# Performance work log

Hardware: AMD Instinct MI355X
Metric: run time of the kernel (lower is better)

The kernel has to match this reference:

```python
import jax, jax.numpy as jnp
import numpy as np

N = 65536   # total nodes
E = 1048576 # total edges (avg degree 16)
B = 512     # graphs in batch
H = 4       # gat1 heads
C = 64      # per-head channels / GNN_HIDDEN


def segment_softmax(logits, seg, num_segments):
    # numerically stable softmax over segments (PyG softmax semantics, eps=1e-16)
    m = jax.ops.segment_max(logits, seg, num_segments=num_segments)
    m = jnp.where(jnp.isfinite(m), m, 0.0)
    e = jnp.exp(logits - m[seg])
    s = jax.ops.segment_sum(e, seg, num_segments=num_segments)
    return e / (s[seg] + 1e-16)


def gat_conv(x, edge_index, edge_attr, W, att_src, att_dst, We, att_edge, bias, heads, out_ch, concat):
    # PyG GATConv with edge_dim, add_self_loops=False
    n = x.shape[0]
    h = (x @ W).reshape(n, heads, out_ch)                 # (N,H,C)
    src, dst = edge_index[0], edge_index[1]
    a_s = jnp.sum(h * att_src, axis=-1)                   # (N,H)
    a_d = jnp.sum(h * att_dst, axis=-1)                   # (N,H)
    he = (edge_attr @ We).reshape(-1, heads, out_ch)      # (E,H,C)
    a_e = jnp.sum(he * att_edge, axis=-1)                 # (E,H)
    alpha = jax.nn.leaky_relu(a_s[src] + a_d[dst] + a_e, negative_slope=0.2)
    alpha = segment_softmax(alpha, dst, n)                # softmax over incoming edges per dst
    out = jax.ops.segment_sum(h[src] * alpha[..., None], dst, num_segments=n)  # (N,H,C)
    out = out.reshape(n, heads * out_ch) if concat else out.mean(axis=1)
    return out + bias


def setup_inputs() -> dict:
    key = jax.random.key(0)
    ks = jax.random.split(key, 24)
    s = 0.05
    d = {}
    d["global_feat"] = jax.random.normal(ks[0], (B, 512), jnp.float32)
    d["x"] = jax.random.normal(ks[1], (N, 13), jnp.float32)
    d["roi_feats"] = jax.random.normal(ks[2], (N, 256), jnp.float32)
    d["edge_index"] = jax.random.randint(ks[3], (2, E), 0, N)
    d["edge_attr"] = jax.random.normal(ks[4], (E, 5), jnp.float32)
    d["batch_vec"] = jnp.sort(jax.random.randint(ks[5], (N,), 0, B))
    # roi_proj / scene_proj
    d["roi_W"] = jax.random.normal(ks[6], (256, 64), jnp.float32) * s
    d["roi_b"] = jnp.zeros((64,), jnp.float32)
    d["scene_W"] = jax.random.normal(ks[7], (512, 128), jnp.float32) * s
    d["scene_b"] = jnp.zeros((128,), jnp.float32)
    d["g1_W"] = jax.random.normal(ks[8], (77, H * C), jnp.float32) * s
    d["g1_att_src"] = jax.random.normal(ks[9], (H, C), jnp.float32) * s
    d["g1_att_dst"] = jax.random.normal(ks[10], (H, C), jnp.float32) * s
    d["g1_We"] = jax.random.normal(ks[11], (5, H * C), jnp.float32) * s
    d["g1_att_edge"] = jax.random.normal(ks[12], (H, C), jnp.float32) * s
    d["g1_bias"] = jnp.zeros((H * C,), jnp.float32)
    # gat2: 256 -> 64, 1 head
    d["g2_W"] = jax.random.normal(ks[13], (H * C, C), jnp.float32) * s
    d["g2_att_src"] = jax.random.normal(ks[14], (1, C), jnp.float32) * s
    d["g2_att_dst"] = jax.random.normal(ks[15], (1, C), jnp.float32) * s
    d["g2_We"] = jax.random.normal(ks[16], (5, C), jnp.float32) * s
    d["g2_att_edge"] = jax.random.normal(ks[17], (1, C), jnp.float32) * s
    d["g2_bias"] = jnp.zeros((C,), jnp.float32)
    # attention pooling gate + classifier
    d["gate_W"] = jax.random.normal(ks[18], (C, 1), jnp.float32) * s
    d["gate_b"] = jnp.zeros((1,), jnp.float32)
    d["cls1_W"] = jax.random.normal(ks[19], (128 + C, 64), jnp.float32) * s
    d["cls1_b"] = jnp.zeros((64,), jnp.float32)
    d["cls2_W"] = jax.random.normal(ks[20], (64, 3), jnp.float32) * s
    d["cls2_b"] = jnp.zeros((3,), jnp.float32)
    return d


def reference(global_feat, x, roi_feats, edge_index, edge_attr, batch_vec,
              roi_W, roi_b, scene_W, scene_b,
              g1_W, g1_att_src, g1_att_dst, g1_We, g1_att_edge, g1_bias,
              g2_W, g2_att_src, g2_att_dst, g2_We, g2_att_edge, g2_bias,
              gate_W, gate_b, cls1_W, cls1_b, cls2_W, cls2_b):
    scene = global_feat @ scene_W + scene_b                       # (B,128)
    vis = jax.nn.relu(roi_feats @ roi_W + roi_b)                  # (N,64)
    h = jnp.concatenate([x, vis], axis=-1)                        # (N,77)
    h = jax.nn.relu(gat_conv(h, edge_index, edge_attr, g1_W, g1_att_src, g1_att_dst, g1_We, g1_att_edge, g1_bias, H, C, True))
    h = gat_conv(h, edge_index, edge_attr, g2_W, g2_att_src, g2_att_dst, g2_We, g2_att_edge, g2_bias, 1, C, False)  # (N,64)
    # GlobalAttention pooling
    gate = segment_softmax((h @ gate_W + gate_b)[:, 0], batch_vec, B)
    rel = jax.ops.segment_sum(gate[:, None] * h, batch_vec, num_segments=B)  # (B,64)
    comb = jnp.concatenate([scene, rel], axis=-1)                 # (B,192)
    hid = jax.nn.relu(comb @ cls1_W + cls1_b)                     # dropout off (eval)
    return hid @ cls2_W + cls2_b                                  # (B,3)
```

## Files before the change

kernel.cpp:

```cpp
#include <hip/hip_runtime.h>

#define N_NODES 65536
#define N_EDGES 1048576
#define NB      512

typedef unsigned short u16;
typedef unsigned int   u32;
typedef unsigned long long u64;

__device__ __forceinline__ float bf2f(u16 u) { return __uint_as_float(((u32)u) << 16); }
__device__ __forceinline__ float lo16(u32 u) { return __uint_as_float(u << 16); }
__device__ __forceinline__ float hi16(u32 u) { return __uint_as_float(u & 0xffff0000u); }
__device__ __forceinline__ u16 f2bf(float f) {
    u32 u = __float_as_uint(f);
    u32 r = (u + 0x7fffu + ((u >> 16) & 1u)) >> 16;
    return (u16)r;
}
__device__ __forceinline__ float wsum(float v) {
    for (int o = 32; o; o >>= 1) v += __shfl_xor(v, o, 64);
    return v;
}
__device__ __forceinline__ float wmax(float v) {
    for (int o = 32; o; o >>= 1) v = fmaxf(v, __shfl_xor(v, o, 64));
    return v;
}

__global__ void k_prep(const float* g1We, const float* g1ae, const float* g2We, const float* g2ae,
                       float* M1, float* M2) {
    int t = threadIdx.x;
    if (t < 20) {
        int j = t >> 2, h = t & 3;
        float s = 0.f;
        for (int c = 0; c < 64; c++) s += g1We[j * 256 + h * 64 + c] * g1ae[h * 64 + c];
        M1[t] = s;
    } else if (t < 25) {
        int j = t - 20;
        float s = 0.f;
        for (int c = 0; c < 64; c++) s += g2We[j * 64 + c] * g2ae[c];
        M2[j] = s;
    }
}

__global__ __launch_bounds__(256) void k_scene(const float* __restrict__ gf, const float* __restrict__ W,
                                               const float* __restrict__ bias, float* __restrict__ scene) {
    int idx = blockIdx.x * 256 + threadIdx.x;
    int b = idx >> 7, j = idx & 127;
    float acc = 0.f;
    for (int k = 0; k < 512; k++) acc += gf[b * 512 + k] * W[k * 128 + j];
    scene[idx] = acc + bias[j];
}

__global__ __launch_bounds__(256) void k_hist(const int* ei, int* cnt) {
    int e = blockIdx.x * 256 + threadIdx.x;
    atomicAdd(&cnt[ei[N_EDGES + e]], 1);
}

__global__ __launch_bounds__(256) void k_scan_blk(const int* __restrict__ cnt, int* __restrict__ pre,
                                                  int* __restrict__ bsum) {
    __shared__ int sd[256];
    int t = threadIdx.x, b = blockIdx.x;
    int base = b * 1024 + t * 4;
    int4 c = *(const int4*)(cnt + base);
    int s = c.x + c.y + c.z + c.w;
    sd[t] = s;
    __syncthreads();
    for (int off = 1; off < 256; off <<= 1) {
        int v = (t >= off) ? sd[t - off] : 0;
        __syncthreads();
        sd[t] += v;
        __syncthreads();
    }
    int excl = sd[t] - s;
    int4 p;
    p.x = excl;
    p.y = excl + c.x;
    p.z = excl + c.x + c.y;
    p.w = excl + c.x + c.y + c.z;
    *(int4*)(pre + base) = p;
    if (t == 255) bsum[b] = sd[255];
}

__global__ __launch_bounds__(64) void k_scan_top(int* bsum) {
    int t = threadIdx.x;
    int v = bsum[t];
    int inc = v;
    for (int off = 1; off < 64; off <<= 1) {
        int u = __shfl_up(inc, off, 64);
        if (t >= off) inc += u;
    }
    bsum[t] = inc - v;
}

__global__ __launch_bounds__(256) void k_scan_fix(const int* __restrict__ pre, const int* __restrict__ bsum,
                                                  int* __restrict__ row_ptr, int* __restrict__ coarse_cur) {
    int i = blockIdx.x * 256 + threadIdx.x;
    int v = pre[i] + bsum[i >> 10];
    row_ptr[i] = v;
    if ((i & 255) == 0) coarse_cur[i >> 8] = v;
    if (i == 0) row_ptr[N_NODES] = N_EDGES;
}

__global__ __launch_bounds__(256) void k_bucket(const int* __restrict__ ei, int* coarse_cur,
                                                u32* __restrict__ bpack, int* __restrict__ bsrc) {
    __shared__ u32 stageP[4096];
    __shared__ int stageS[4096];
    __shared__ int bcnt[256], bscan[256], boff[256], gbase[256];
    int t = threadIdx.x;
    int e0 = blockIdx.x * 4096;
    bcnt[t] = 0;
    __syncthreads();
    int dreg[16], sreg[16];
    for (int it = 0; it < 16; it++) {
        int e = e0 + it * 256 + t;
        int dd = ei[N_EDGES + e];
        dreg[it] = dd;
        sreg[it] = ei[e];
        atomicAdd(&bcnt[dd >> 8], 1);
    }
    __syncthreads();
    int v = bcnt[t];
    bscan[t] = v;
    __syncthreads();
    for (int off = 1; off < 256; off <<= 1) {
        int u = (t >= off) ? bscan[t - off] : 0;
        __syncthreads();
        bscan[t] += u;
        __syncthreads();
    }
    boff[t] = bscan[t] - v;
    gbase[t] = v ? atomicAdd(&coarse_cur[t], v) : 0;
    __syncthreads();
    for (int it = 0; it < 16; it++) {
        int e = e0 + it * 256 + t;
        int b = dreg[it] >> 8;
        int pos = atomicAdd(&boff[b], 1);
        stageP[pos] = ((u32)e << 12) | (u32)(dreg[it] & 255);
        stageS[pos] = sreg[it];
    }
    __syncthreads();
    for (int idx = t; idx < 4096; idx += 256) {
        int lo = 0, hi = 255;
        while (lo < hi) { int mid = (lo + hi) >> 1; if (bscan[mid] > idx) hi = mid; else lo = mid + 1; }
        int b = lo;
        int g = gbase[b] + (idx - (bscan[b] - bcnt[b]));
        bpack[g] = stageP[idx];
        bsrc[g] = stageS[idx];
    }
}

__global__ __launch_bounds__(256) void k_sortb(const u32* __restrict__ bpack, const int* __restrict__ bsrc,
                                               const int* __restrict__ row_ptr,
                                               int* __restrict__ eord, int* __restrict__ ssrc) {
    __shared__ int cur[256];
    int t = threadIdx.x, b = blockIdx.x;
    int nbase = b * 256;
    cur[t] = row_ptr[nbase + t];
    __syncthreads();
    int beg = row_ptr[nbase];
    int end = row_ptr[nbase + 256];
    for (int i = beg + t; i < end; i += 256) {
        u32 wd = bpack[i];
        int src = bsrc[i];
        int d8 = wd & 255;
        int pos = atomicAdd(&cur[d8], 1);
        eord[pos] = (int)(wd >> 12);
        ssrc[pos] = src;
    }
}

__global__ __launch_bounds__(256) void k_payload(const int* __restrict__ eord, const float* __restrict__ ea,
                                                 const float* __restrict__ M1, const float* __restrict__ M2,
                                                 float* __restrict__ a1es, float* __restrict__ a2es) {
    int pos = blockIdx.x * 256 + threadIdx.x;
    int e = eord[pos];
    float v[5];
    for (int j = 0; j < 5; j++) v[j] = ea[(size_t)e * 5 + j];
    float4 o;
    o.x = v[0]*M1[0]  + v[1]*M1[4]  + v[2]*M1[8]  + v[3]*M1[12] + v[4]*M1[16];
    o.y = v[0]*M1[1]  + v[1]*M1[5]  + v[2]*M1[9]  + v[3]*M1[13] + v[4]*M1[17];
    o.z = v[0]*M1[2]  + v[1]*M1[6]  + v[2]*M1[10] + v[3]*M1[14] + v[4]*M1[18];
    o.w = v[0]*M1[3]  + v[1]*M1[7]  + v[2]*M1[11] + v[3]*M1[15] + v[4]*M1[19];
    *(float4*)(a1es + (size_t)pos * 4) = o;
    a2es[pos] = v[0]*M2[0] + v[1]*M2[1] + v[2]*M2[2] + v[3]*M2[3] + v[4]*M2[4];
}

__global__ __launch_bounds__(256) void k_vis(const float* __restrict__ A, const float* __restrict__ W,
                                             const float* __restrict__ bias, float* __restrict__ out) {
    __shared__ float At[64][68];
    __shared__ float Wl[64][68];
    int t = threadIdx.x;
    int n0 = blockIdx.x * 64;
    int cg = t & 15, rg = t >> 4;
    int sr = t >> 2, scs = (t & 3) * 16;
    float acc[4][4];
    for (int i = 0; i < 4; i++) for (int j = 0; j < 4; j++) acc[i][j] = 0.f;
    for (int kc = 0; kc < 4; kc++) {
        __syncthreads();
        const float* ap = A + (size_t)(n0 + sr) * 256 + kc * 64 + scs;
        float4 q0 = *(const float4*)ap, q1 = *(const float4*)(ap + 4);
        float4 q2 = *(const float4*)(ap + 8), q3 = *(const float4*)(ap + 12);
        At[scs + 0][sr] = q0.x;  At[scs + 1][sr] = q0.y;  At[scs + 2][sr] = q0.z;  At[scs + 3][sr] = q0.w;
        At[scs + 4][sr] = q1.x;  At[scs + 5][sr] = q1.y;  At[scs + 6][sr] = q1.z;  At[scs + 7][sr] = q1.w;
        At[scs + 8][sr] = q2.x;  At[scs + 9][sr] = q2.y;  At[scs + 10][sr] = q2.z; At[scs + 11][sr] = q2.w;
        At[scs + 12][sr] = q3.x; At[scs + 13][sr] = q3.y; At[scs + 14][sr] = q3.z; At[scs + 15][sr] = q3.w;
        const float* wp = W + (size_t)(kc * 64 + sr) * 64 + scs;
        *(float4*)&Wl[sr][scs + 0]  = *(const float4*)wp;
        *(float4*)&Wl[sr][scs + 4]  = *(const float4*)(wp + 4);
        *(float4*)&Wl[sr][scs + 8]  = *(const float4*)(wp + 8);
        *(float4*)&Wl[sr][scs + 12] = *(const float4*)(wp + 12);
        __syncthreads();
        for (int k = 0; k < 64; k++) {
            float4 a4 = *(const float4*)&At[k][rg * 4];
            float4 w4 = *(const float4*)&Wl[k][cg * 4];
            acc[0][0] += a4.x * w4.x; acc[0][1] += a4.x * w4.y; acc[0][2] += a4.x * w4.z; acc[0][3] += a4.x * w4.w;
            acc[1][0] += a4.y * w4.x; acc[1][1] += a4.y * w4.y; acc[1][2] += a4.y * w4.z; acc[1][3] += a4.y * w4.w;
            acc[2][0] += a4.z * w4.x; acc[2][1] += a4.z * w4.y; acc[2][2] += a4.z * w4.z; acc[2][3] += a4.z * w4.w;
            acc[3][0] += a4.w * w4.x; acc[3][1] += a4.w * w4.y; acc[3][2] += a4.w * w4.z; acc[3][3] += a4.w * w4.w;
        }
    }
    float4 bb = *(const float4*)(bias + cg * 4);
    for (int i = 0; i < 4; i++) {
        float4 o;
        o.x = fmaxf(acc[i][0] + bb.x, 0.f);
        o.y = fmaxf(acc[i][1] + bb.y, 0.f);
        o.z = fmaxf(acc[i][2] + bb.z, 0.f);
        o.w = fmaxf(acc[i][3] + bb.w, 0.f);
        *(float4*)(out + (size_t)(n0 + rg * 4 + i) * 64 + cg * 4) = o;
    }
}

__global__ __launch_bounds__(256) void k_h2(const u16* __restrict__ A, const float* __restrict__ W,
                                            u16* __restrict__ out) {
    __shared__ float At[64][68];
    __shared__ float Wl[64][68];
    int t = threadIdx.x;
    int n0 = blockIdx.x * 64;
    int cg = t & 15, rg = t >> 4;
    int sr = t >> 2, scs = (t & 3) * 16;
    float acc[4][4];
    for (int i = 0; i < 4; i++) for (int j = 0; j < 4; j++) acc[i][j] = 0.f;
    for (int kc = 0; kc < 4; kc++) {
        __syncthreads();
        const u16* ap = A + (size_t)(n0 + sr) * 256 + kc * 64 + scs;
        uint4 u0 = *(const uint4*)ap;
        uint4 u1 = *(const uint4*)(ap + 8);
        At[scs + 0][sr] = lo16(u0.x);  At[scs + 1][sr] = hi16(u0.x);
        At[scs + 2][sr] = lo16(u0.y);  At[scs + 3][sr] = hi16(u0.y);
        At[scs + 4][sr] = lo16(u0.z);  At[scs + 5][sr] = hi16(u0.z);
        At[scs + 6][sr] = lo16(u0.w);  At[scs + 7][sr] = hi16(u0.w);
        At[scs + 8][sr] = lo16(u1.x);  At[scs + 9][sr] = hi16(u1.x);
        At[scs + 10][sr] = lo16(u1.y); At[scs + 11][sr] = hi16(u1.y);
        At[scs + 12][sr] = lo16(u1.z); At[scs + 13][sr] = hi16(u1.z);
        At[scs + 14][sr] = lo16(u1.w); At[scs + 15][sr] = hi16(u1.w);
        const float* wp = W + (size_t)(kc * 64 + sr) * 64 + scs;
        *(float4*)&Wl[sr][scs + 0]  = *(const float4*)wp;
        *(float4*)&Wl[sr][scs + 4]  = *(const float4*)(wp + 4);
        *(float4*)&Wl[sr][scs + 8]  = *(const float4*)(wp + 8);
        *(float4*)&Wl[sr][scs + 12] = *(const float4*)(wp + 12);
        __syncthreads();
        for (int k = 0; k < 64; k++) {
            float4 a4 = *(const float4*)&At[k][rg * 4];
            float4 w4 = *(const float4*)&Wl[k][cg * 4];
            acc[0][0] += a4.x * w4.x; acc[0][1] += a4.x * w4.y; acc[0][2] += a4.x * w4.z; acc[0][3] += a4.x * w4.w;
            acc[1][0] += a4.y * w4.x; acc[1][1] += a4.y * w4.y; acc[1][2] += a4.y * w4.z; acc[1][3] += a4.y * w4.w;
            acc[2][0] += a4.z * w4.x; acc[2][1] += a4.z * w4.y; acc[2][2] += a4.z * w4.z; acc[2][3] += a4.z * w4.w;
            acc[3][0] += a4.w * w4.x; acc[3][1] += a4.w * w4.y; acc[3][2] += a4.w * w4.z; acc[3][3] += a4.w * w4.w;
        }
    }
    u32* outu = (u32*)out;
    for (int i = 0; i < 4; i++) {
        uint2 pk;
        pk.x = (u32)f2bf(acc[i][0]) | ((u32)f2bf(acc[i][1]) << 16);
        pk.y = (u32)f2bf(acc[i][2]) | ((u32)f2bf(acc[i][3]) << 16);
        *(uint2*)(outu + (size_t)(n0 + rg * 4 + i) * 32 + cg * 2) = pk;
    }
}

__global__ __launch_bounds__(256) void k_h1(const float* __restrict__ x, const float* __restrict__ vis,
                                            const float* __restrict__ g1W, u16* __restrict__ h1) {
    __shared__ float At[77][36];
    __shared__ float Wl[77][132];
    int t = threadIdx.x, ch = blockIdx.y;
    int n0 = blockIdx.x * 32;
    int cg = t & 31, rg = t >> 5;
    for (int idx = t; idx < 9856; idx += 256) {
        int k = idx >> 7, c = idx & 127;
        Wl[k][c] = g1W[(size_t)k * 256 + ch * 128 + c];
    }
    for (int idx = t; idx < 2464; idx += 256) {
        int r = idx / 77, k = idx - r * 77;
        At[k][r] = (k < 13) ? x[(size_t)(n0 + r) * 13 + k] : vis[(size_t)(n0 + r) * 64 + (k - 13)];
    }
    __syncthreads();
    float acc[4][4];
    for (int i = 0; i < 4; i++) for (int j = 0; j < 4; j++) acc[i][j] = 0.f;
    for (int k = 0; k < 77; k++) {
        float4 a4 = *(const float4*)&At[k][rg * 4];
        float4 w4 = *(const float4*)&Wl[k][cg * 4];
        acc[0][0] += a4.x * w4.x; acc[0][1] += a4.x * w4.y; acc[0][2] += a4.x * w4.z; acc[0][3] += a4.x * w4.w;
        acc[1][0] += a4.y * w4.x; acc[1][1] += a4.y * w4.y; acc[1][2] += a4.y * w4.z; acc[1][3] += a4.y * w4.w;
        acc[2][0] += a4.z * w4.x; acc[2][1] += a4.z * w4.y; acc[2][2] += a4.z * w4.z; acc[2][3] += a4.z * w4.w;
        acc[3][0] += a4.w * w4.x; acc[3][1] += a4.w * w4.y; acc[3][2] += a4.w * w4.z; acc[3][3] += a4.w * w4.w;
    }
    for (int i = 0; i < 4; i++) {
        uint2 pk;
        pk.x = (u32)f2bf(acc[i][0]) | ((u32)f2bf(acc[i][1]) << 16);
        pk.y = (u32)f2bf(acc[i][2]) | ((u32)f2bf(acc[i][3]) << 16);
        *(uint2*)(h1 + (size_t)(n0 + rg * 4 + i) * 256 + ch * 128 + cg * 4) = pk;
    }
}

__global__ __launch_bounds__(256) void k_a1(const u16* __restrict__ h1, const float* __restrict__ as_,
                                            const float* __restrict__ ad_, float* a1s, float* a1d) {
    int t = threadIdx.x;
    int w = t >> 6, L = t & 63;
    float4 as4 = *(const float4*)(as_ + 4 * L);
    float4 ad4 = *(const float4*)(ad_ + 4 * L);
    int base = (blockIdx.x * 4 + w) * 16;
    for (int j = 0; j < 16; j++) {
        int n = base + j;
        uint2 u = *((const uint2*)(h1 + (size_t)n * 256) + L);
        float v0 = lo16(u.x), v1 = hi16(u.x), v2 = lo16(u.y), v3 = hi16(u.y);
        float ps = v0 * as4.x + v1 * as4.y + v2 * as4.z + v3 * as4.w;
        float pd = v0 * ad4.x + v1 * ad4.y + v2 * ad4.z + v3 * ad4.w;
        for (int o = 1; o < 16; o <<= 1) { ps += __shfl_xor(ps, o, 64); pd += __shfl_xor(pd, o, 64); }
        if ((L & 15) == 0) {
            a1s[n * 4 + (L >> 4)] = ps;
            a1d[n * 4 + (L >> 4)] = pd;
        }
    }
}

__global__ __launch_bounds__(256) void k_a2(const u16* __restrict__ h2b, const float* __restrict__ as_,
                                            const float* __restrict__ ad_, float* a2s, float* a2d) {
    int t = threadIdx.x;
    int w = t >> 6, lane = t & 63;
    int n = blockIdx.x * 4 + w;
    float v = bf2f(h2b[(size_t)n * 64 + lane]);
    float ps = wsum(v * as_[lane]);
    float pd = wsum(v * ad_[lane]);
    if (lane == 0) { a2s[n] = ps; a2d[n] = pd; }
}

__global__ __launch_bounds__(256) void k_soft1(const int* __restrict__ row_ptr, const int* __restrict__ ssrc,
                                               const float* __restrict__ a1s, const float* __restrict__ a1d,
                                               const float* __restrict__ a1es, float* __restrict__ w1) {
    int t = threadIdx.x;
    int wv = t >> 6, L = t & 63;
    int n = blockIdx.x * 4 + wv;
    int h = L >> 4, j = L & 15;
    int beg = row_ptr[n], deg = row_ptr[n + 1] - beg;
    if (deg == 0) return;
    float adn = a1d[n * 4 + h];
    float m = -3.0e38f, s = 0.f;
    for (int i = j; i < deg; i += 16) {
        int pos = beg + i;
        float l = a1s[ssrc[pos] * 4 + h] + adn + a1es[(size_t)pos * 4 + h];
        l = (l > 0.f) ? l : 0.2f * l;
        if (l > m) { s = s * __expf(m - l) + 1.f; m = l; }
        else       { s += __expf(l - m); }
    }
    for (int o = 1; o < 16; o <<= 1) {
        float mo = __shfl_xor(m, o, 64), so = __shfl_xor(s, o, 64);
        float M = fmaxf(m, mo);
        s = s * __expf(m - M) + so * __expf(mo - M);
        m = M;
    }
    float inv = 1.f / (s + 1e-16f);
    for (int i = j; i < deg; i += 16) {
        int pos = beg + i;
        float l = a1s[ssrc[pos] * 4 + h] + adn + a1es[(size_t)pos * 4 + h];
        l = (l > 0.f) ? l : 0.2f * l;
        w1[(size_t)pos * 4 + h] = __expf(l - m) * inv;
    }
}

__global__ __launch_bounds__(256) void k_gath1(const int* __restrict__ row_ptr, const int* __restrict__ ssrc,
                                               const float* __restrict__ w1, const u16* __restrict__ h1,
                                               const float* __restrict__ bias, u16* __restrict__ out1) {
    int t = threadIdx.x;
    int wv = t >> 6, L = t & 63;
    int n = blockIdx.x * 4 + wv;
    int beg = row_ptr[n], deg = row_ptr[n + 1] - beg;
    int halfE = L >> 5;
    int L32 = L & 31;
    int hd = L32 >> 3;
    float acc[8];
    #pragma unroll
    for (int j = 0; j < 8; j++) acc[j] = 0.f;
    int last = beg + deg - 1;
    for (int i = 0; i < deg; i += 4) {
        int iA = i + halfE, iB = i + 2 + halfE;
        int pA = beg + iA, pB = beg + iB;
        bool vA = iA < deg, vB = iB < deg;
        int cA = vA ? pA : last, cB = vB ? pB : last;
        int sA = ssrc[cA], sB = ssrc[cB];
        float wA = vA ? w1[(size_t)cA * 4 + hd] : 0.f;
        float wB = vB ? w1[(size_t)cB * 4 + hd] : 0.f;
        uint4 uA = *((const uint4*)(h1 + (size_t)sA * 256) + L32);
        uint4 uB = *((const uint4*)(h1 + (size_t)sB * 256) + L32);
        acc[0] += wA * lo16(uA.x) + wB * lo16(uB.x);
        acc[1] += wA * hi16(uA.x) + wB * hi16(uB.x);
        acc[2] += wA * lo16(uA.y) + wB * lo16(uB.y);
        acc[3] += wA * hi16(uA.y) + wB * hi16(uB.y);
        acc[4] += wA * lo16(uA.z) + wB * lo16(uB.z);
        acc[5] += wA * hi16(uA.z) + wB * hi16(uB.z);
        acc[6] += wA * lo16(uA.w) + wB * lo16(uB.w);
        acc[7] += wA * hi16(uA.w) + wB * hi16(uB.w);
    }
    #pragma unroll
    for (int j = 0; j < 8; j++) acc[j] += __shfl_xor(acc[j], 32, 64);
    if (halfE == 0) {
        float4 b0 = *(const float4*)(bias + 8 * L32);
        float4 b1 = *(const float4*)(bias + 8 * L32 + 4);
        uint4 pk;
        pk.x = (u32)f2bf(fmaxf(acc[0] + b0.x, 0.f)) | ((u32)f2bf(fmaxf(acc[1] + b0.y, 0.f)) << 16);
        pk.y = (u32)f2bf(fmaxf(acc[2] + b0.z, 0.f)) | ((u32)f2bf(fmaxf(acc[3] + b0.w, 0.f)) << 16);
        pk.z = (u32)f2bf(fmaxf(acc[4] + b1.x, 0.f)) | ((u32)f2bf(fmaxf(acc[5] + b1.y, 0.f)) << 16);
        pk.w = (u32)f2bf(fmaxf(acc[6] + b1.z, 0.f)) | ((u32)f2bf(fmaxf(acc[7] + b1.w, 0.f)) << 16);
        *((uint4*)(out1 + (size_t)n * 256) + L32) = pk;
    }
}

__global__ __launch_bounds__(256) void k_soft2(const int* __restrict__ row_ptr, const int* __restrict__ ssrc,
                                               const float* __restrict__ a2s, const float* __restrict__ a2d,
                                               const float* __restrict__ a2es, float* __restrict__ w2) {
    int t = threadIdx.x;
    int wv = t >> 6, L = t & 63;
    int g = L >> 4, j = L & 15;
    int n = blockIdx.x * 16 + wv * 4 + g;
    int beg = row_ptr[n], deg = row_ptr[n + 1] - beg;
    if (deg == 0) return;
    float adn = a2d[n];
    float m = -3.0e38f, s = 0.f;
    for (int i = j; i < deg; i += 16) {
        int pos = beg + i;
        float l = a2s[ssrc[pos]] + adn + a2es[pos];
        l = (l > 0.f) ? l : 0.2f * l;
        if (l > m) { s = s * __expf(m - l) + 1.f; m = l; }
        else       { s += __expf(l - m); }
    }
    for (int o = 1; o < 16; o <<= 1) {
        float mo = __shfl_xor(m, o, 64), so = __shfl_xor(s, o, 64);
        float M = fmaxf(m, mo);
        s = s * __expf(m - M) + so * __expf(mo - M);
        m = M;
    }
    float inv = 1.f / (s + 1e-16f);
    for (int i = j; i < deg; i += 16) {
        int pos = beg + i;
        float l = a2s[ssrc[pos]] + adn + a2es[pos];
        l = (l > 0.f) ? l : 0.2f * l;
        w2[pos] = __expf(l - m) * inv;
    }
}

__global__ __launch_bounds__(256) void k_gath2(const int* __restrict__ row_ptr, const int* __restrict__ ssrc,
                                               const float* __restrict__ w2, const u16* __restrict__ h2b,
                                               const float* __restrict__ bias, float* __restrict__ hfin) {
    int t = threadIdx.x;
    int wv = t >> 6, L = t & 63;
    int n = blockIdx.x * 4 + wv;
    int beg = row_ptr[n], deg = row_ptr[n + 1] - beg;
    int halfE = L >> 5;
    int L32 = L & 31;
    float a0 = 0.f, a1v = 0.f;
    int last = beg + deg - 1;
    const u32* h2u = (const u32*)h2b;
    for (int i = 0; i < deg; i += 4) {
        int iA = i + halfE, iB = i + 2 + halfE;
        int pA = beg + iA, pB = beg + iB;
        bool vA = iA < deg, vB = iB < deg;
        int cA = vA ? pA : last, cB = vB ? pB : last;
        int sA = ssrc[cA], sB = ssrc[cB];
        float wA = vA ? w2[cA] : 0.f;
        float wB = vB ? w2[cB] : 0.f;
        u32 uA = h2u[(size_t)sA * 32 + L32];
        u32 uB = h2u[(size_t)sB * 32 + L32];
        a0  += wA * lo16(uA) + wB * lo16(uB);
        a1v += wA * hi16(uA) + wB * hi16(uB);
    }
    a0  += __shfl_xor(a0, 32, 64);
    a1v += __shfl_xor(a1v, 32, 64);
    if (halfE == 0) {
        float2 o;
        o.x = a0  + bias[2 * L32];
        o.y = a1v + bias[2 * L32 + 1];
        *(float2*)(hfin + (size_t)n * 64 + 2 * L32) = o;
    }
}

__global__ __launch_bounds__(64) void k_pool(const int* __restrict__ bvec, const float* __restrict__ hf,
                                             const float* gateW, const float* gateb,
                                             const float* __restrict__ scene,
                                             const float* c1W, const float* c1b,
                                             const float* c2W, const float* c2b,
                                             float* __restrict__ outp) {
    int b = blockIdx.x, lane = threadIdx.x;
    __shared__ float gwl[64], se[64], comb[192], hid[64];
    gwl[lane] = gateW[lane];
    __syncthreads();
    int s0, s1;
    { int lo = 0, hi = N_NODES; while (lo < hi) { int mid = (lo + hi) >> 1; if (bvec[mid] < b) lo = mid + 1; else hi = mid; } s0 = lo; }
    { int lo = 0, hi = N_NODES; while (lo < hi) { int mid = (lo + hi) >> 1; if (bvec[mid] < b + 1) lo = mid + 1; else hi = mid; } s1 = lo; }
    float gb = gateb[0];
    float m = -3.0e38f, ssum = 0.f, acc = 0.f;
    for (int cs = s0; cs < s1; cs += 64) {
        int cnt = min(64, s1 - cs);
        float l = -3.0e38f;
        if (lane < cnt) {
            int n = cs + lane;
            float d = 0.f;
            for (int i = 0; i < 64; i++) d += hf[(size_t)n * 64 + i] * gwl[i];
            l = d + gb;
        }
        float cm = wmax(l);
        float newm = fmaxf(m, cm);
        float rsc = __expf(m - newm);
        float e = (lane < cnt) ? __expf(l - newm) : 0.f;
        float es = wsum(e);
        ssum = ssum * rsc + es;
        se[lane] = e;
        __syncthreads();
        float a2 = 0.f;
        for (int i = 0; i < cnt; i++) a2 += se[i] * hf[(size_t)(cs + i) * 64 + lane];
        acc = acc * rsc + a2;
        __syncthreads();
        m = newm;
    }
    float rel = acc / (ssum + 1e-16f);
    comb[lane] = scene[b * 128 + lane];
    comb[64 + lane] = scene[b * 128 + 64 + lane];
    comb[128 + lane] = rel;
    __syncthreads();
    float hj = 0.f;
    for (int k = 0; k < 192; k++) hj += comb[k] * c1W[k * 64 + lane];
    hj += c1b[lane];
    hid[lane] = fmaxf(hj, 0.f);
    __syncthreads();
    if (lane < 3) {
        float o = 0.f;
        for (int k = 0; k < 64; k++) o += hid[k] * c2W[k * 3 + lane];
        o += c2b[lane];
        outp[b * 3 + lane] = o;
    }
}

extern "C" void kernel_launch(void* const* d_in, const int* in_sizes, int n_in,
                              void* d_out, int out_size, void* d_ws, size_t ws_size,
                              hipStream_t stream) {
    (void)in_sizes; (void)n_in; (void)out_size; (void)ws_size;
    const float* gf     = (const float*)d_in[0];
    const float* x      = (const float*)d_in[1];
    const float* roi    = (const float*)d_in[2];
    const int*   ei     = (const int*)d_in[3];
    const float* ea     = (const float*)d_in[4];
    const int*   bvec   = (const int*)d_in[5];
    const float* roiW   = (const float*)d_in[6];
    const float* roib   = (const float*)d_in[7];
    const float* sceneW = (const float*)d_in[8];
    const float* sceneb = (const float*)d_in[9];
    const float* g1W    = (const float*)d_in[10];
    const float* g1as   = (const float*)d_in[11];
    const float* g1ad   = (const float*)d_in[12];
    const float* g1We   = (const float*)d_in[13];
    const float* g1ae   = (const float*)d_in[14];
    const float* g1b    = (const float*)d_in[15];
    const float* g2W    = (const float*)d_in[16];
    const float* g2as   = (const float*)d_in[17];
    const float* g2ad   = (const float*)d_in[18];
    const float* g2We   = (const float*)d_in[19];
    const float* g2ae   = (const float*)d_in[20];
    const float* g2b    = (const float*)d_in[21];
    const float* gateW  = (const float*)d_in[22];
    const float* gateb  = (const float*)d_in[23];
    const float* c1W    = (const float*)d_in[24];
    const float* c1b    = (const float*)d_in[25];
    const float* c2W    = (const float*)d_in[26];
    const float* c2b    = (const float*)d_in[27];

    char* w = (char*)d_ws;
    size_t o = 0;
    auto nxt = [&](size_t bytes) -> char* {
        char* p = w + o;
        o += (bytes + 255) & ~(size_t)255;
        return p;
    };
    float* scene  = (float*)nxt((size_t)NB * 128 * 4);
    float* M1     = (float*)nxt(80);
    float* M2     = (float*)nxt(32);
    int* cnt      = (int*)nxt((size_t)N_NODES * 4);
    int* pre      = (int*)nxt((size_t)N_NODES * 4);
    int* bsum     = (int*)nxt(64 * 4);
    int* row_ptr  = (int*)nxt((size_t)(N_NODES + 1) * 4);
    int* coarse   = (int*)nxt(256 * 4);
    u32* bpack    = (u32*)nxt((size_t)N_EDGES * 4);
    int* bsrc     = (int*)nxt((size_t)N_EDGES * 4);
    int* eord     = (int*)nxt((size_t)N_EDGES * 4);
    int* ssrc     = (int*)nxt((size_t)N_EDGES * 4);
    float* a1es   = (float*)nxt((size_t)N_EDGES * 16);
    float* a2es   = (float*)nxt((size_t)N_EDGES * 4);
    float* visbuf = (float*)nxt((size_t)N_NODES * 64 * 4);
    u16* h1       = (u16*)nxt((size_t)N_NODES * 256 * 2);
    u16* out1     = (u16*)nxt((size_t)N_NODES * 256 * 2);
    float* w1buf  = (float*)nxt((size_t)N_EDGES * 16);
    float* hfin   = (float*)nxt((size_t)N_NODES * 64 * 4);
    float* a1s    = (float*)nxt((size_t)N_NODES * 16);
    float* a1d    = (float*)nxt((size_t)N_NODES * 16);
    float* a2s    = (float*)nxt((size_t)N_NODES * 4);
    float* a2d    = (float*)nxt((size_t)N_NODES * 4);

    float* vis = visbuf;
    float* w2  = visbuf;
    float* w1  = w1buf;
    u16*   h2b = (u16*)w1buf;

    hipMemsetAsync(cnt, 0, (size_t)N_NODES * 4, stream);
    k_prep<<<1, 32, 0, stream>>>(g1We, g1ae, g2We, g2ae, M1, M2);
    k_scene<<<(NB * 128) / 256, 256, 0, stream>>>(gf, sceneW, sceneb, scene);
    k_hist<<<N_EDGES / 256, 256, 0, stream>>>(ei, cnt);
    k_scan_blk<<<64, 256, 0, stream>>>(cnt, pre, bsum);
    k_scan_top<<<1, 64, 0, stream>>>(bsum);
    k_scan_fix<<<N_NODES / 256, 256, 0, stream>>>(pre, bsum, row_ptr, coarse);
    k_bucket<<<256, 256, 0, stream>>>(ei, coarse, bpack, bsrc);
    k_sortb<<<256, 256, 0, stream>>>(bpack, bsrc, row_ptr, eord, ssrc);
    k_payload<<<N_EDGES / 256, 256, 0, stream>>>(eord, ea, M1, M2, a1es, a2es);
    k_vis<<<N_NODES / 64, 256, 0, stream>>>(roi, roiW, roib, vis);
    k_h1<<<dim3(N_NODES / 32, 2), 256, 0, stream>>>(x, vis, g1W, h1);
    k_a1<<<N_NODES / 64, 256, 0, stream>>>(h1, g1as, g1ad, a1s, a1d);
    k_soft1<<<N_NODES / 4, 256, 0, stream>>>(row_ptr, ssrc, a1s, a1d, a1es, w1);
    k_gath1<<<N_NODES / 4, 256, 0, stream>>>(row_ptr, ssrc, w1, h1, g1b, out1);
    k_h2<<<N_NODES / 64, 256, 0, stream>>>(out1, g2W, h2b);
    k_a2<<<N_NODES / 4, 256, 0, stream>>>(h2b, g2as, g2ad, a2s, a2d);
    k_soft2<<<N_NODES / 16, 256, 0, stream>>>(row_ptr, ssrc, a2s, a2d, a2es, w2);
    k_gath2<<<N_NODES / 4, 256, 0, stream>>>(row_ptr, ssrc, w2, h2b, g2b, hfin);
    k_pool<<<NB, 64, 0, stream>>>(bvec, hfin, gateW, gateb, scene, c1W, c1b, c2W, c2b, (float*)d_out);
}
```

Baseline: 640.9 us.

## Fuse attention dot into h2 GEMM, cache logits in softmax, unroll gathers

The second-layer source and destination attention scores are now computed inside the k_h2 GEMM epilogue from the fp32 accumulators, which removes the separate k_a2 launch and its re-read of h2. Both softmax kernels store the leaky-relu logits in the output buffer during the first pass and read them back in the second, instead of re-gathering a_s[src] and the edge terms. Both gather kernels now process four edges per iteration instead of two, putting more independent loads in flight. The attention scores now come from unrounded fp32 values rather than bf16 ones, and the gather loops use more registers.

Result: faster. 624.8 us (-2.5%).

```diff
diff --git a/kernel.cpp b/kernel.cpp
--- a/kernel.cpp
+++ b/kernel.cpp
@@ -230,7 +230,9 @@
 }
 
 __global__ __launch_bounds__(256) void k_h2(const u16* __restrict__ A, const float* __restrict__ W,
-                                            u16* __restrict__ out) {
+                                            const float* __restrict__ as_, const float* __restrict__ ad_,
+                                            u16* __restrict__ out, float* __restrict__ a2s,
+                                            float* __restrict__ a2d) {
     __shared__ float At[64][68];
     __shared__ float Wl[64][68];
     int t = threadIdx.x;
@@ -274,6 +276,18 @@
         pk.y = (u32)f2bf(acc[i][2]) | ((u32)f2bf(acc[i][3]) << 16);
         *(uint2*)(outu + (size_t)(n0 + rg * 4 + i) * 32 + cg * 2) = pk;
     }
+    float4 as4 = *(const float4*)(as_ + cg * 4);
+    float4 ad4 = *(const float4*)(ad_ + cg * 4);
+    #pragma unroll
+    for (int i = 0; i < 4; i++) {
+        float ps = acc[i][0] * as4.x + acc[i][1] * as4.y + acc[i][2] * as4.z + acc[i][3] * as4.w;
+        float pd = acc[i][0] * ad4.x + acc[i][1] * ad4.y + acc[i][2] * ad4.z + acc[i][3] * ad4.w;
+        for (int o = 1; o < 16; o <<= 1) { ps += __shfl_xor(ps, o, 64); pd += __shfl_xor(pd, o, 64); }
+        if (cg == 0) {
+            a2s[n0 + rg * 4 + i] = ps;
+            a2d[n0 + rg * 4 + i] = pd;
+        }
+    }
 }
 
 __global__ __launch_bounds__(256) void k_h1(const float* __restrict__ x, const float* __restrict__ vis,
@@ -331,17 +345,6 @@
     }
 }
 
-__global__ __launch_bounds__(256) void k_a2(const u16* __restrict__ h2b, const float* __restrict__ as_,
-                                            const float* __restrict__ ad_, float* a2s, float* a2d) {
-    int t = threadIdx.x;
-    int w = t >> 6, lane = t & 63;
-    int n = blockIdx.x * 4 + w;
-    float v = bf2f(h2b[(size_t)n * 64 + lane]);
-    float ps = wsum(v * as_[lane]);
-    float pd = wsum(v * ad_[lane]);
-    if (lane == 0) { a2s[n] = ps; a2d[n] = pd; }
-}
-
 __global__ __launch_bounds__(256) void k_soft1(const int* __restrict__ row_ptr, const int* __restrict__ ssrc,
                                                const float* __restrict__ a1s, const float* __restrict__ a1d,
                                                const float* __restrict__ a1es, float* __restrict__ w1) {
@@ -357,6 +360,7 @@
         int pos = beg + i;
         float l = a1s[ssrc[pos] * 4 + h] + adn + a1es[(size_t)pos * 4 + h];
         l = (l > 0.f) ? l : 0.2f * l;
+        w1[(size_t)pos * 4 + h] = l;
         if (l > m) { s = s * __expf(m - l) + 1.f; m = l; }
         else       { s += __expf(l - m); }
     }
@@ -369,8 +373,7 @@
     float inv = 1.f / (s + 1e-16f);
     for (int i = j; i < deg; i += 16) {
         int pos = beg + i;
-        float l = a1s[ssrc[pos] * 4 + h] + adn + a1es[(size_t)pos * 4 + h];
-        l = (l > 0.f) ? l : 0.2f * l;
+        float l = w1[(size_t)pos * 4 + h];
         w1[(size_t)pos * 4 + h] = __expf(l - m) * inv;
     }
 }
@@ -389,24 +392,28 @@
     #pragma unroll
     for (int j = 0; j < 8; j++) acc[j] = 0.f;
     int last = beg + deg - 1;
-    for (int i = 0; i < deg; i += 4) {
-        int iA = i + halfE, iB = i + 2 + halfE;
-        int pA = beg + iA, pB = beg + iB;
-        bool vA = iA < deg, vB = iB < deg;
-        int cA = vA ? pA : last, cB = vB ? pB : last;
-        int sA = ssrc[cA], sB = ssrc[cB];
+    for (int i = 0; i < deg; i += 8) {
+        int iA = i + halfE, iB = i + 2 + halfE, iC = i + 4 + halfE, iD = i + 6 + halfE;
+        bool vA = iA < deg, vB = iB < deg, vC = iC < deg, vD = iD < deg;
+        int cA = vA ? beg + iA : last, cB = vB ? beg + iB : last;
+        int cC = vC ? beg + iC : last, cD = vD ? beg + iD : last;
+        int sA = ssrc[cA], sB = ssrc[cB], sC = ssrc[cC], sD = ssrc[cD];
         float wA = vA ? w1[(size_t)cA * 4 + hd] : 0.f;
         float wB = vB ? w1[(size_t)cB * 4 + hd] : 0.f;
+        float wC = vC ? w1[(size_t)cC * 4 + hd] : 0.f;
+        float wD = vD ? w1[(size_t)cD * 4 + hd] : 0.f;
         uint4 uA = *((const uint4*)(h1 + (size_t)sA * 256) + L32);
         uint4 uB = *((const uint4*)(h1 + (size_t)sB * 256) + L32);
-        acc[0] += wA * lo16(uA.x) + wB * lo16(uB.x);
-        acc[1] += wA * hi16(uA.x) + wB * hi16(uB.x);
-        acc[2] += wA * lo16(uA.y) + wB * lo16(uB.y);
-        acc[3] += wA * hi16(uA.y) + wB * hi16(uB.y);
-        acc[4] += wA * lo16(uA.z) + wB * lo16(uB.z);
-        acc[5] += wA * hi16(uA.z) + wB * hi16(uB.z);
-        acc[6] += wA * lo16(uA.w) + wB * lo16(uB.w);
-        acc[7] += wA * hi16(uA.w) + wB * hi16(uB.w);
+        uint4 uC = *((const uint4*)(h1 + (size_t)sC * 256) + L32);
+        uint4 uD = *((const uint4*)(h1 + (size_t)sD * 256) + L32);
+        acc[0] += wA * lo16(uA.x) + wB * lo16(uB.x) + wC * lo16(uC.x) + wD * lo16(uD.x);
+        acc[1] += wA * hi16(uA.x) + wB * hi16(uB.x) + wC * hi16(uC.x) + wD * hi16(uD.x);
+        acc[2] += wA * lo16(uA.y) + wB * lo16(uB.y) + wC * lo16(uC.y) + wD * lo16(uD.y);
+        acc[3] += wA * hi16(uA.y) + wB * hi16(uB.y) + wC * hi16(uC.y) + wD * hi16(uD.y);
+        acc[4] += wA * lo16(uA.z) + wB * lo16(uB.z) + wC * lo16(uC.z) + wD * lo16(uD.z);
+        acc[5] += wA * hi16(uA.z) + wB * hi16(uB.z) + wC * hi16(uC.z) + wD * hi16(uD.z);
+        acc[6] += wA * lo16(uA.w) + wB * lo16(uB.w) + wC * lo16(uC.w) + wD * lo16(uD.w);
+        acc[7] += wA * hi16(uA.w) + wB * hi16(uB.w) + wC * hi16(uC.w) + wD * hi16(uD.w);
     }
     #pragma unroll
     for (int j = 0; j < 8; j++) acc[j] += __shfl_xor(acc[j], 32, 64);
@@ -437,6 +444,7 @@
         int pos = beg + i;
         float l = a2s[ssrc[pos]] + adn + a2es[pos];
         l = (l > 0.f) ? l : 0.2f * l;
+        w2[pos] = l;
         if (l > m) { s = s * __expf(m - l) + 1.f; m = l; }
         else       { s += __expf(l - m); }
     }
@@ -449,8 +457,7 @@
     float inv = 1.f / (s + 1e-16f);
     for (int i = j; i < deg; i += 16) {
         int pos = beg + i;
-        float l = a2s[ssrc[pos]] + adn + a2es[pos];
-        l = (l > 0.f) ? l : 0.2f * l;
+        float l = w2[pos];
         w2[pos] = __expf(l - m) * inv;
     }
 }
@@ -467,18 +474,22 @@
     float a0 = 0.f, a1v = 0.f;
     int last = beg + deg - 1;
     const u32* h2u = (const u32*)h2b;
-    for (int i = 0; i < deg; i += 4) {
-        int iA = i + halfE, iB = i + 2 + halfE;
-        int pA = beg + iA, pB = beg + iB;
-        bool vA = iA < deg, vB = iB < deg;
-        int cA = vA ? pA : last, cB = vB ? pB : last;
-        int sA = ssrc[cA], sB = ssrc[cB];
+    for (int i = 0; i < deg; i += 8) {
+        int iA = i + halfE, iB = i + 2 + halfE, iC = i + 4 + halfE, iD = i + 6 + halfE;
+        bool vA = iA < deg, vB = iB < deg, vC = iC < deg, vD = iD < deg;
+        int cA = vA ? beg + iA : last, cB = vB ? beg + iB : last;
+        int cC = vC ? beg + iC : last, cD = vD ? beg + iD : last;
+        int sA = ssrc[cA], sB = ssrc[cB], sC = ssrc[cC], sD = ssrc[cD];
         float wA = vA ? w2[cA] : 0.f;
         float wB = vB ? w2[cB] : 0.f;
+        float wC = vC ? w2[cC] : 0.f;
+        float wD = vD ? w2[cD] : 0.f;
         u32 uA = h2u[(size_t)sA * 32 + L32];
         u32 uB = h2u[(size_t)sB * 32 + L32];
-        a0  += wA * lo16(uA) + wB * lo16(uB);
-        a1v += wA * hi16(uA) + wB * hi16(uB);
+        u32 uC = h2u[(size_t)sC * 32 + L32];
+        u32 uD = h2u[(size_t)sD * 32 + L32];
+        a0  += wA * lo16(uA) + wB * lo16(uB) + wC * lo16(uC) + wD * lo16(uD);
+        a1v += wA * hi16(uA) + wB * hi16(uB) + wC * hi16(uC) + wD * hi16(uD);
     }
     a0  += __shfl_xor(a0, 32, 64);
     a1v += __shfl_xor(a1v, 32, 64);
@@ -630,8 +641,7 @@
     k_a1<<<N_NODES / 64, 256, 0, stream>>>(h1, g1as, g1ad, a1s, a1d);
     k_soft1<<<N_NODES / 4, 256, 0, stream>>>(row_ptr, ssrc, a1s, a1d, a1es, w1);
     k_gath1<<<N_NODES / 4, 256, 0, stream>>>(row_ptr, ssrc, w1, h1, g1b, out1);
-    k_h2<<<N_NODES / 64, 256, 0, stream>>>(out1, g2W, h2b);
-    k_a2<<<N_NODES / 4, 256, 0, stream>>>(h2b, g2as, g2ad, a2s, a2d);
+    k_h2<<<N_NODES / 64, 256, 0, stream>>>(out1, g2W, g2as, g2ad, h2b, a2s, a2d);
     k_soft2<<<N_NODES / 16, 256, 0, stream>>>(row_ptr, ssrc, a2s, a2d, a2es, w2);
     k_gath2<<<N_NODES / 4, 256, 0, stream>>>(row_ptr, ssrc, w2, h2b, g2b, hfin);
     k_pool<<<NB, 64, 0, stream>>>(bvec, hfin, gateW, gateb, scene, c1W, c1b, c2W, c2b, (float*)d_out);
```
